# Kernel tuning notes

Hardware: AMD Instinct MI355X
Metric: run time of the kernel (lower is better)

## Reference

```python
import jax, jax.numpy as jnp
import numpy as np

D_MODEL = 1024
N_HEADS = 16
DH = (D_MODEL // N_HEADS) // 2  # depth // 2 = 32
B, S = 4, 2048


def setup_inputs() -> dict:
    key = jax.random.key(0)
    ks = jax.random.split(key, 8)
    scale_in = 1.0
    q = jax.random.normal(ks[0], (B, S, D_MODEL), dtype=jnp.float32)
    k = jax.random.normal(ks[1], (B, S, D_MODEL), dtype=jnp.float32)
    v = jax.random.normal(ks[2], (B, S, D_MODEL), dtype=jnp.float32)
    # Per-head projection weights stacked over the head axis (glorot-ish init)
    w_std = (2.0 / (D_MODEL + DH)) ** 0.5
    Wq = jax.random.normal(ks[3], (N_HEADS, D_MODEL, DH), dtype=jnp.float32) * w_std
    Wk = jax.random.normal(ks[4], (N_HEADS, D_MODEL, DH), dtype=jnp.float32) * w_std
    Wv = jax.random.normal(ks[5], (N_HEADS, D_MODEL, DH), dtype=jnp.float32) * w_std
    wo_std = (2.0 / (N_HEADS * DH + D_MODEL)) ** 0.5
    Wo = jax.random.normal(ks[6], (N_HEADS * DH, D_MODEL), dtype=jnp.float32) * wo_std
    return {"q": q, "k": k, "v": v, "Wq": Wq, "Wk": Wk, "Wv": Wv, "Wo": Wo}


def reference(q, k, v, Wq, Wk, Wv, Wo):
    # NOTE: source scales by d_model**-0.5 (not head_dim**-0.5)
    scale = D_MODEL ** (-0.5)
    Q = jnp.einsum("bsd,hde->bhse", q, Wq)   # [B,H,S,DH]
    K = jnp.einsum("btd,hde->bhte", k, Wk)
    V = jnp.einsum("btd,hde->bhte", v, Wv)
    attn = jnp.einsum("bhse,bhte->bhst", Q, K) * scale  # [B,H,S,S]
    attn = jax.nn.softmax(attn, axis=-1)
    x = jnp.einsum("bhst,bhte->bhse", attn, V)  # [B,H,S,DH]
    # concat heads along feature dim (head order = concat order in source)
    x = jnp.transpose(x, (0, 2, 1, 3)).reshape(q.shape[0], q.shape[1], N_HEADS * DH)
    return x @ Wo  # [B,S,D_MODEL]; dropout is identity (training=False)
```

## Files before the change

kernel.cpp:

```cpp
#include <hip/hip_runtime.h>
#include <hip/hip_bf16.h>

typedef __attribute__((ext_vector_type(8))) short short8;
typedef __attribute__((ext_vector_type(4))) float f32x4;
typedef __attribute__((ext_vector_type(4))) float fv4;
typedef __attribute__((ext_vector_type(4))) unsigned int u32x4;

#define MFMA16(a, b, c) __builtin_amdgcn_mfma_f32_16x16x32_bf16((a), (b), (c), 0, 0, 0)

typedef const __attribute__((address_space(1))) unsigned int gu32;
typedef __attribute__((address_space(3))) unsigned int lu32;

__device__ __forceinline__ short f2b(float f) {
  unsigned int x = __builtin_bit_cast(unsigned int, f);
  x += 0x7fffu + ((x >> 16) & 1u);
  return (short)(x >> 16);
}

__device__ __forceinline__ unsigned int cvtpk(float lo, float hi) {
  unsigned int r;
  asm("v_cvt_pk_bf16_f32 %0, %1, %2" : "=v"(r) : "v"(lo), "v"(hi));
  return r;
}

#define hexp2(x) __builtin_amdgcn_exp2f(x)

__global__ void prep_weights(const float* __restrict__ Wq, const float* __restrict__ Wk,
                             const float* __restrict__ Wv, const float* __restrict__ Wo,
                             short* __restrict__ WqT, short* __restrict__ WkT,
                             short* __restrict__ WvT, short* __restrict__ WoT) {
  const float SC2 = 0.045084220027780106f;
  int idx = blockIdx.x * 256 + threadIdx.x;
  if (idx < 3 * 512 * 1024) {
    int wsel = idx >> 19;
    int rem = idx & ((1 << 19) - 1);
    int n = rem >> 10;
    int d = rem & 1023;
    const float* W = (wsel == 0) ? Wq : ((wsel == 1) ? Wk : Wv);
    short* WT = (wsel == 0) ? WqT : ((wsel == 1) ? WkT : WvT);
    float v = W[(n >> 5) * (1024 * 32) + d * 32 + (n & 31)];
    if (wsel == 0) v *= SC2;
    WT[n * 1024 + d] = f2b(v);
  } else {
    int idx2 = idx - 3 * 512 * 1024;
    int n = idx2 >> 9;
    int kk = idx2 & 511;
    WoT[n * 512 + kk] = f2b(Wo[kk * 1024 + n]);
  }
}

#define BM 128
#define BN 128
#define BK 64
#define LDK 72

template <int K, bool A_F32>
__device__ __forceinline__ void gemm_acc(const void* __restrict__ Av,
                                         const short* __restrict__ BT,
                                         int bm0, int bn0,
                                         short As[BM][LDK], short Bs[BN][LDK],
                                         f32x4 acc[4][4]) {
  const int tid = threadIdx.x;
  const int lane = tid & 63;
  const int l15 = lane & 15, g = lane >> 4;
  const int w = tid >> 6;
  const int wm = (w >> 1) * 64, wn = (w & 1) * 64;
  const int r8 = tid >> 3;
  const int c8 = (tid & 7) * 8;

  for (int k0 = 0; k0 < K; k0 += BK) {
    short8 a_st[4], b_st[4];
    if constexpr (A_F32) {
      const float* A = (const float*)Av;
#pragma unroll
      for (int p = 0; p < 4; ++p) {
        const float* src = A + (size_t)(bm0 + r8 + p * 32) * K + k0 + c8;
        fv4 f0 = *(const fv4*)src;
        fv4 f1 = *(const fv4*)(src + 4);
        u32x4 wv;
        wv[0] = cvtpk(f0[0], f0[1]);
        wv[1] = cvtpk(f0[2], f0[3]);
        wv[2] = cvtpk(f1[0], f1[1]);
        wv[3] = cvtpk(f1[2], f1[3]);
        a_st[p] = __builtin_bit_cast(short8, wv);
      }
    } else {
      const short* A = (const short*)Av;
#pragma unroll
      for (int p = 0; p < 4; ++p)
        a_st[p] = *(const short8*)(A + (size_t)(bm0 + r8 + p * 32) * K + k0 + c8);
    }
#pragma unroll
    for (int p = 0; p < 4; ++p)
      b_st[p] = *(const short8*)(BT + (size_t)(bn0 + r8 + p * 32) * K + k0 + c8);

    __syncthreads();
#pragma unroll
    for (int p = 0; p < 4; ++p) *(short8*)(&As[r8 + p * 32][c8]) = a_st[p];
#pragma unroll
    for (int p = 0; p < 4; ++p) *(short8*)(&Bs[r8 + p * 32][c8]) = b_st[p];
    __syncthreads();

#pragma unroll
    for (int kk = 0; kk < 2; ++kk) {
      short8 af[4], bfr[4];
#pragma unroll
      for (int mf = 0; mf < 4; ++mf)
        af[mf] = *(const short8*)(&As[wm + mf * 16 + l15][kk * 32 + g * 8]);
#pragma unroll
      for (int nf = 0; nf < 4; ++nf)
        bfr[nf] = *(const short8*)(&Bs[wn + nf * 16 + l15][kk * 32 + g * 8]);
#pragma unroll
      for (int mf = 0; mf < 4; ++mf)
#pragma unroll
        for (int nf = 0; nf < 4; ++nf)
          acc[mf][nf] = MFMA16(af[mf], bfr[nf], acc[mf][nf]);
    }
  }
}

__global__ __launch_bounds__(256, 2) void proj_gemm(
    const float* __restrict__ q, const float* __restrict__ k, const float* __restrict__ v,
    const short* __restrict__ WqT, const short* __restrict__ WkT, const short* __restrict__ WvT,
    short* __restrict__ Qb, short* __restrict__ Kb, short* __restrict__ Vtb) {
  __shared__ short As[BM][LDK];
  __shared__ short Bs[BN][LDK];
  const int id = blockIdx.x;
  const int bm = id & 63;
  const int r = id >> 6;
  const int bn = r & 3;
  const int z = r >> 2;
  const float* A = (z == 0) ? q : ((z == 1) ? k : v);
  const short* BT = (z == 0) ? WqT : ((z == 1) ? WkT : WvT);
  const int bm0 = bm * BM, bn0 = bn * BN;

  f32x4 zf = {0.f, 0.f, 0.f, 0.f};
  f32x4 acc[4][4];
#pragma unroll
  for (int a = 0; a < 4; ++a)
#pragma unroll
    for (int bq = 0; bq < 4; ++bq) acc[a][bq] = zf;

  gemm_acc<1024, true>(A, BT, bm0, bn0, As, Bs, acc);

  const int lane = threadIdx.x & 63;
  const int l15 = lane & 15, g = lane >> 4;
  const int w = threadIdx.x >> 6;
  const int wm = (w >> 1) * 64, wn = (w & 1) * 64;
#pragma unroll
  for (int mf = 0; mf < 4; ++mf)
#pragma unroll
    for (int nf = 0; nf < 4; ++nf)
#pragma unroll
      for (int i = 0; i < 4; ++i) {
        int row = bm0 + wm + mf * 16 + g * 4 + i;
        int col = bn0 + wn + nf * 16 + l15;
        int bb = row >> 11, ss = row & 2047;
        int hh = col >> 5, ee = col & 31;
        short val = f2b(acc[mf][nf][i]);
        if (z == 2)
          Vtb[((size_t)(bb * 16 + hh) * 32 + ee) * 2048 + ss] = val;
        else if (z == 1)
          Kb[((size_t)(bb * 16 + hh) * 2048 + ss) * 32 + ee] = val;
        else
          Qb[((size_t)(bb * 16 + hh) * 2048 + ss) * 32 + ee] = val;
      }
}

__global__ __launch_bounds__(256, 2) void out_gemm(const short* __restrict__ X,
                                                   const short* __restrict__ WoT,
                                                   float* __restrict__ out) {
  __shared__ short As[BM][LDK];
  __shared__ short Bs[BN][LDK];
  const int id = blockIdx.x;
  const int bm0 = (id & 63) * BM, bn0 = (id >> 6) * BN;
  f32x4 zf = {0.f, 0.f, 0.f, 0.f};
  f32x4 acc[4][4];
#pragma unroll
  for (int a = 0; a < 4; ++a)
#pragma unroll
    for (int bq = 0; bq < 4; ++bq) acc[a][bq] = zf;

  gemm_acc<512, false>(X, WoT, bm0, bn0, As, Bs, acc);

  const int lane = threadIdx.x & 63;
  const int l15 = lane & 15, g = lane >> 4;
  const int w = threadIdx.x >> 6;
  const int wm = (w >> 1) * 64, wn = (w & 1) * 64;
#pragma unroll
  for (int mf = 0; mf < 4; ++mf)
#pragma unroll
    for (int nf = 0; nf < 4; ++nf)
#pragma unroll
      for (int i = 0; i < 4; ++i) {
        int row = bm0 + wm + mf * 16 + g * 4 + i;
        int col = bn0 + wn + nf * 16 + l15;
        out[(size_t)row * 1024 + col] = acc[mf][nf][i];
      }
}

__device__ __forceinline__ void qk_half(short8 k0, short8 k1, short8 k2, short8 k3,
                                        short8 qf, const f32x4& zf,
                                        short8& pf0, short8& pf1) {
  f32x4 s0 = MFMA16(k0, qf, zf);
  f32x4 s1 = MFMA16(k1, qf, zf);
  f32x4 s2 = MFMA16(k2, qf, zf);
  f32x4 s3 = MFMA16(k3, qf, zf);
#pragma unroll
  for (int i = 0; i < 4; ++i) {
    s0[i] = hexp2(s0[i]);
    s1[i] = hexp2(s1[i]);
    s2[i] = hexp2(s2[i]);
    s3[i] = hexp2(s3[i]);
  }
  u32x4 w0, w1;
  w0[0] = cvtpk(s0[0], s0[1]);
  w0[1] = cvtpk(s0[2], s0[3]);
  w0[2] = cvtpk(s1[0], s1[1]);
  w0[3] = cvtpk(s1[2], s1[3]);
  w1[0] = cvtpk(s2[0], s2[1]);
  w1[1] = cvtpk(s2[2], s2[3]);
  w1[2] = cvtpk(s3[0], s3[1]);
  w1[3] = cvtpk(s3[2], s3[3]);
  pf0 = __builtin_bit_cast(short8, w0);
  pf1 = __builtin_bit_cast(short8, w1);
}

__global__ __launch_bounds__(256, 4) void attn(const short* __restrict__ Qb,
                                               const short* __restrict__ Kb,
                                               const short* __restrict__ Vtb,
                                               short* __restrict__ X) {
  __shared__ short KV[2][2][2048];
  const int tid = threadIdx.x;
  const int lane = tid & 63;
  const int w = tid >> 6;
  const int l15 = lane & 15, g = lane >> 4;
  const int id = blockIdx.x;
  const int bh = id & 63;
  const int qblk = id >> 6;
  const int bb = bh >> 4, hh = bh & 15;
  const int q0 = qblk * 128 + w * 32;

  const short* Qp = Qb + ((size_t)bh * 2048 + q0) * 32;
  const short* Kp = Kb + (size_t)bh * 2048 * 32;
  const short* Vp = Vtb + (size_t)bh * 32 * 2048;

  short8 qfA = *(const short8*)(Qp + l15 * 32 + g * 8);
  short8 qfB = *(const short8*)(Qp + (16 + l15) * 32 + g * 8);

  const int kbase = 8 * (l15 >> 2) + (l15 & 3);
  const int koff = (w & 1) * 4 + (w >> 1) * 32;
  const int vrow = (w >> 1) * 16;
  const int vcol = (w & 1) * 32;
  const short* Ksrc0 = Kp + (size_t)(kbase + koff) * 32 + g * 8;
  const short* Vsrc0 = Vp + (size_t)(l15 + vrow) * 2048 + vcol + g * 8;

  f32x4 zf = {0.f, 0.f, 0.f, 0.f};
  f32x4 o_loA = zf, o_hiA = zf, o_loB = zf, o_hiB = zf;
  f32x4 accLA = zf, accLB = zf;
  u32x4 ones_u = {0x3F803F80u, 0x3F803F80u, 0x3F803F80u, 0x3F803F80u};
  const short8 ones = __builtin_bit_cast(short8, ones_u);

#define STAGE(b, t0)                                                        \
  {                                                                         \
    __builtin_amdgcn_global_load_lds((gu32*)(Ksrc0 + (size_t)(t0) * 32),    \
                                     (lu32*)&KV[b][0][w * 512], 16, 0, 0);  \
    __builtin_amdgcn_global_load_lds((gu32*)(Vsrc0 + (t0)),                 \
                                     (lu32*)&KV[b][1][w * 512], 16, 0, 0);  \
  }

#define BODY(b)                                                       \
  {                                                                   \
    short8 k0 = *(const short8*)(&KV[b][0][0 * 512 + lane * 8]);      \
    short8 k1 = *(const short8*)(&KV[b][0][1 * 512 + lane * 8]);      \
    short8 k2 = *(const short8*)(&KV[b][0][2 * 512 + lane * 8]);      \
    short8 k3 = *(const short8*)(&KV[b][0][3 * 512 + lane * 8]);      \
    short8 vlo0 = *(const short8*)(&KV[b][1][0 * 512 + lane * 8]);    \
    short8 vlo1 = *(const short8*)(&KV[b][1][1 * 512 + lane * 8]);    \
    short8 vhi0 = *(const short8*)(&KV[b][1][2 * 512 + lane * 8]);    \
    short8 vhi1 = *(const short8*)(&KV[b][1][3 * 512 + lane * 8]);    \
    short8 pfA0, pfA1, pfB0, pfB1;                                    \
    qk_half(k0, k1, k2, k3, qfA, zf, pfA0, pfA1);                     \
    qk_half(k0, k1, k2, k3, qfB, zf, pfB0, pfB1);                     \
    __builtin_amdgcn_s_setprio(1);                                    \
    accLA = MFMA16(pfA0, ones, accLA);                                \
    accLA = MFMA16(pfA1, ones, accLA);                                \
    accLB = MFMA16(pfB0, ones, accLB);                                \
    accLB = MFMA16(pfB1, ones, accLB);                                \
    o_loA = MFMA16(pfA0, vlo0, o_loA);                                \
    o_loA = MFMA16(pfA1, vlo1, o_loA);                                \
    o_hiA = MFMA16(pfA0, vhi0, o_hiA);                                \
    o_hiA = MFMA16(pfA1, vhi1, o_hiA);                                \
    o_loB = MFMA16(pfB0, vlo0, o_loB);                                \
    o_loB = MFMA16(pfB1, vlo1, o_loB);                                \
    o_hiB = MFMA16(pfB0, vhi0, o_hiB);                                \
    o_hiB = MFMA16(pfB1, vhi1, o_hiB);                                \
    __builtin_amdgcn_s_setprio(0);                                    \
  }

  STAGE(0, 0);
  __syncthreads();
  for (int t0 = 0; t0 < 2048; t0 += 128) {
    STAGE(1, t0 + 64);
    BODY(0);
    __syncthreads();
    if (t0 + 128 < 2048) {
      STAGE(0, t0 + 128);
    }
    BODY(1);
    __syncthreads();
  }
#undef STAGE
#undef BODY

#pragma unroll
  for (int i = 0; i < 4; ++i) {
    float invA = 1.0f / accLA[i];
    float invB = 1.0f / accLB[i];
    int ssA = q0 + 4 * g + i;
    size_t baseA = ((size_t)bb * 2048 + ssA) * 512 + hh * 32;
    X[baseA + l15] = f2b(o_loA[i] * invA);
    X[baseA + 16 + l15] = f2b(o_hiA[i] * invA);
    size_t baseB = baseA + (size_t)16 * 512;
    X[baseB + l15] = f2b(o_loB[i] * invB);
    X[baseB + 16 + l15] = f2b(o_hiB[i] * invB);
  }
}

extern "C" void kernel_launch(void* const* d_in, const int* in_sizes, int n_in,
                              void* d_out, int out_size, void* d_ws, size_t ws_size,
                              hipStream_t stream) {
  const float* q = (const float*)d_in[0];
  const float* k = (const float*)d_in[1];
  const float* v = (const float*)d_in[2];
  const float* Wq = (const float*)d_in[3];
  const float* Wk = (const float*)d_in[4];
  const float* Wv = (const float*)d_in[5];
  const float* Wo = (const float*)d_in[6];

  char* ws = (char*)d_ws;
  const size_t MB = 1u << 20;
  short* WqT = (short*)(ws + 0 * MB);
  short* WkT = (short*)(ws + 1 * MB);
  short* WvT = (short*)(ws + 2 * MB);
  short* WoT = (short*)(ws + 3 * MB);
  short* Qb  = (short*)(ws + 4 * MB);
  short* Kb  = (short*)(ws + 12 * MB);
  short* Vtb = (short*)(ws + 20 * MB);
  short* Xb  = (short*)(ws + 28 * MB);

  prep_weights<<<8192, 256, 0, stream>>>(Wq, Wk, Wv, Wo, WqT, WkT, WvT, WoT);
  proj_gemm<<<768, 256, 0, stream>>>(q, k, v, WqT, WkT, WvT, Qb, Kb, Vtb);
  attn<<<1024, 256, 0, stream>>>(Qb, Kb, Vtb, Xb);
  out_gemm<<<512, 256, 0, stream>>>(Xb, WoT, (float*)d_out);
}
```

Baseline: 121.5 us.

## Stage projection and output GEMM tiles via direct global-to-LDS loads with XOR swizzle

```diff
diff --git a/kernel.cpp b/kernel.cpp
--- a/kernel.cpp
+++ b/kernel.cpp
@@ -49,82 +49,16 @@
   }
 }
 
-#define BM 128
-#define BN 128
-#define BK 64
-#define LDK 72
-
-template <int K, bool A_F32>
-__device__ __forceinline__ void gemm_acc(const void* __restrict__ Av,
-                                         const short* __restrict__ BT,
-                                         int bm0, int bn0,
-                                         short As[BM][LDK], short Bs[BN][LDK],
-                                         f32x4 acc[4][4]) {
-  const int tid = threadIdx.x;
-  const int lane = tid & 63;
-  const int l15 = lane & 15, g = lane >> 4;
-  const int w = tid >> 6;
-  const int wm = (w >> 1) * 64, wn = (w & 1) * 64;
-  const int r8 = tid >> 3;
-  const int c8 = (tid & 7) * 8;
-
-  for (int k0 = 0; k0 < K; k0 += BK) {
-    short8 a_st[4], b_st[4];
-    if constexpr (A_F32) {
-      const float* A = (const float*)Av;
-#pragma unroll
-      for (int p = 0; p < 4; ++p) {
-        const float* src = A + (size_t)(bm0 + r8 + p * 32) * K + k0 + c8;
-        fv4 f0 = *(const fv4*)src;
-        fv4 f1 = *(const fv4*)(src + 4);
-        u32x4 wv;
-        wv[0] = cvtpk(f0[0], f0[1]);
-        wv[1] = cvtpk(f0[2], f0[3]);
-        wv[2] = cvtpk(f1[0], f1[1]);
-        wv[3] = cvtpk(f1[2], f1[3]);
-        a_st[p] = __builtin_bit_cast(short8, wv);
-      }
-    } else {
-      const short* A = (const short*)Av;
-#pragma unroll
-      for (int p = 0; p < 4; ++p)
-        a_st[p] = *(const short8*)(A + (size_t)(bm0 + r8 + p * 32) * K + k0 + c8);
-    }
-#pragma unroll
-    for (int p = 0; p < 4; ++p)
-      b_st[p] = *(const short8*)(BT + (size_t)(bn0 + r8 + p * 32) * K + k0 + c8);
-
-    __syncthreads();
-#pragma unroll
-    for (int p = 0; p < 4; ++p) *(short8*)(&As[r8 + p * 32][c8]) = a_st[p];
-#pragma unroll
-    for (int p = 0; p < 4; ++p) *(short8*)(&Bs[r8 + p * 32][c8]) = b_st[p];
-    __syncthreads();
-
-#pragma unroll
-    for (int kk = 0; kk < 2; ++kk) {
-      short8 af[4], bfr[4];
-#pragma unroll
-      for (int mf = 0; mf < 4; ++mf)
-        af[mf] = *(const short8*)(&As[wm + mf * 16 + l15][kk * 32 + g * 8]);
-#pragma unroll
-      for (int nf = 0; nf < 4; ++nf)
-        bfr[nf] = *(const short8*)(&Bs[wn + nf * 16 + l15][kk * 32 + g * 8]);
-#pragma unroll
-      for (int mf = 0; mf < 4; ++mf)
-#pragma unroll
-        for (int nf = 0; nf < 4; ++nf)
-          acc[mf][nf] = MFMA16(af[mf], bfr[nf], acc[mf][nf]);
-    }
-  }
-}
-
-__global__ __launch_bounds__(256, 2) void proj_gemm(
+__global__ __launch_bounds__(256, 3) void proj_gemm(
     const float* __restrict__ q, const float* __restrict__ k, const float* __restrict__ v,
     const short* __restrict__ WqT, const short* __restrict__ WkT, const short* __restrict__ WvT,
     short* __restrict__ Qb, short* __restrict__ Kb, short* __restrict__ Vtb) {
-  __shared__ short As[BM][LDK];
-  __shared__ short Bs[BN][LDK];
+  __shared__ char smem[49152];
+  const int tid = threadIdx.x;
+  const int lane = tid & 63;
+  const int w = tid >> 6;
+  const int l15 = lane & 15, g = lane >> 4;
+  const int wm = (w >> 1) * 64, wn = (w & 1) * 64;
   const int id = blockIdx.x;
   const int bm = id & 63;
   const int r = id >> 6;
@@ -132,7 +66,12 @@
   const int z = r >> 2;
   const float* A = (z == 0) ? q : ((z == 1) ? k : v);
   const short* BT = (z == 0) ? WqT : ((z == 1) ? WkT : WvT);
-  const int bm0 = bm * BM, bn0 = bn * BN;
+  const int bm0 = bm * 128, bn0 = bn * 128;
+
+  const int arow = lane >> 4;
+  const int au = lane & 15;
+  const int brow = lane >> 3;
+  const int bu = lane & 7;
 
   f32x4 zf = {0.f, 0.f, 0.f, 0.f};
   f32x4 acc[4][4];
@@ -141,12 +80,56 @@
 #pragma unroll
     for (int bq = 0; bq < 4; ++bq) acc[a][bq] = zf;
 
-  gemm_acc<1024, true>(A, BT, bm0, bn0, As, Bs, acc);
-
-  const int lane = threadIdx.x & 63;
-  const int l15 = lane & 15, g = lane >> 4;
-  const int w = threadIdx.x >> 6;
-  const int wm = (w >> 1) * 64, wn = (w & 1) * 64;
+  for (int k0 = 0; k0 < 1024; k0 += 64) {
+#pragma unroll
+    for (int i = 0; i < 8; ++i) {
+      int row = 32 * w + 4 * i + arow;
+      int u = au ^ (row & 7);
+      __builtin_amdgcn_global_load_lds(
+          (gu32*)(A + (size_t)(bm0 + row) * 1024 + k0 + 4 * u),
+          (lu32*)(smem + w * 8192 + i * 1024), 16, 0, 0);
+    }
+#pragma unroll
+    for (int i = 0; i < 4; ++i) {
+      int row = 32 * w + 8 * i + brow;
+      int u = bu ^ (row & 7);
+      __builtin_amdgcn_global_load_lds(
+          (gu32*)(BT + (size_t)(bn0 + row) * 1024 + k0 + 8 * u),
+          (lu32*)(smem + 32768 + w * 4096 + i * 1024), 16, 0, 0);
+    }
+    __syncthreads();
+
+#pragma unroll
+    for (int kk = 0; kk < 2; ++kk) {
+      short8 af[4], bfr[4];
+#pragma unroll
+      for (int mf = 0; mf < 4; ++mf) {
+        int row = wm + mf * 16 + l15;
+        int u0 = 8 * kk + 2 * g;
+        fv4 a0 = *(const fv4*)(smem + row * 256 + ((u0 ^ (row & 7)) * 16));
+        fv4 a1 = *(const fv4*)(smem + row * 256 + (((u0 + 1) ^ (row & 7)) * 16));
+        u32x4 wv;
+        wv[0] = cvtpk(a0[0], a0[1]);
+        wv[1] = cvtpk(a0[2], a0[3]);
+        wv[2] = cvtpk(a1[0], a1[1]);
+        wv[3] = cvtpk(a1[2], a1[3]);
+        af[mf] = __builtin_bit_cast(short8, wv);
+      }
+#pragma unroll
+      for (int nf = 0; nf < 4; ++nf) {
+        int row = wn + nf * 16 + l15;
+        int c = 4 * kk + g;
+        bfr[nf] = *(const short8*)(smem + 32768 + row * 128 + ((c ^ (row & 7)) * 16));
+      }
+#pragma unroll
+      for (int mf = 0; mf < 4; ++mf)
+#pragma unroll
+        for (int nf = 0; nf < 4; ++nf)
+          acc[mf][nf] = MFMA16(af[mf], bfr[nf], acc[mf][nf]);
+    }
+    __syncthreads();
+  }
+
 #pragma unroll
   for (int mf = 0; mf < 4; ++mf)
 #pragma unroll
@@ -170,10 +153,18 @@
 __global__ __launch_bounds__(256, 2) void out_gemm(const short* __restrict__ X,
                                                    const short* __restrict__ WoT,
                                                    float* __restrict__ out) {
-  __shared__ short As[BM][LDK];
-  __shared__ short Bs[BN][LDK];
+  __shared__ char smem[32768];
+  const int tid = threadIdx.x;
+  const int lane = tid & 63;
+  const int w = tid >> 6;
+  const int l15 = lane & 15, g = lane >> 4;
+  const int wm = (w >> 1) * 64, wn = (w & 1) * 64;
   const int id = blockIdx.x;
-  const int bm0 = (id & 63) * BM, bn0 = (id >> 6) * BN;
+  const int bm0 = (id & 63) * 128, bn0 = (id >> 6) * 128;
+
+  const int brow = lane >> 3;
+  const int bu = lane & 7;
+
   f32x4 zf = {0.f, 0.f, 0.f, 0.f};
   f32x4 acc[4][4];
 #pragma unroll
@@ -181,12 +172,44 @@
 #pragma unroll
     for (int bq = 0; bq < 4; ++bq) acc[a][bq] = zf;
 
-  gemm_acc<512, false>(X, WoT, bm0, bn0, As, Bs, acc);
-
-  const int lane = threadIdx.x & 63;
-  const int l15 = lane & 15, g = lane >> 4;
-  const int w = threadIdx.x >> 6;
-  const int wm = (w >> 1) * 64, wn = (w & 1) * 64;
+  for (int k0 = 0; k0 < 512; k0 += 64) {
+#pragma unroll
+    for (int i = 0; i < 4; ++i) {
+      int row = 32 * w + 8 * i + brow;
+      int u = bu ^ (row & 7);
+      __builtin_amdgcn_global_load_lds(
+          (gu32*)(X + (size_t)(bm0 + row) * 512 + k0 + 8 * u),
+          (lu32*)(smem + w * 4096 + i * 1024), 16, 0, 0);
+      __builtin_amdgcn_global_load_lds(
+          (gu32*)(WoT + (size_t)(bn0 + row) * 512 + k0 + 8 * u),
+          (lu32*)(smem + 16384 + w * 4096 + i * 1024), 16, 0, 0);
+    }
+    __syncthreads();
+
+#pragma unroll
+    for (int kk = 0; kk < 2; ++kk) {
+      short8 af[4], bfr[4];
+#pragma unroll
+      for (int mf = 0; mf < 4; ++mf) {
+        int row = wm + mf * 16 + l15;
+        int c = 4 * kk + g;
+        af[mf] = *(const short8*)(smem + row * 128 + ((c ^ (row & 7)) * 16));
+      }
+#pragma unroll
+      for (int nf = 0; nf < 4; ++nf) {
+        int row = wn + nf * 16 + l15;
+        int c = 4 * kk + g;
+        bfr[nf] = *(const short8*)(smem + 16384 + row * 128 + ((c ^ (row & 7)) * 16));
+      }
+#pragma unroll
+      for (int mf = 0; mf < 4; ++mf)
+#pragma unroll
+        for (int nf = 0; nf < 4; ++nf)
+          acc[mf][nf] = MFMA16(af[mf], bfr[nf], acc[mf][nf]);
+    }
+    __syncthreads();
+  }
+
 #pragma unroll
   for (int mf = 0; mf < 4; ++mf)
 #pragma unroll
```

New measurement: 123.1 us. No clear change (+1.3%).
